# Kernel tuning notes

Hardware: AMD Instinct MI355X
Metric: run time of the kernel (lower is better)

## Reference

```python
import jax, jax.numpy as jnp
import numpy as np

T, NINP, NSTATE, NCH, NLAYER, NCLASS = 8192, 128, 1024, 4, 3, 10
GH = NSTATE // NCH  # per-channel GRU hidden size
EPS = 1e-5


def setup_inputs() -> dict:
    key = jax.random.key(0)
    ks = jax.random.split(key, 32)
    rn = lambda k, shape, scale: (jax.random.normal(k, shape, jnp.float32) * scale)
    he = lambda k, shape: rn(k, shape, (2.0 / shape[-1]) ** 0.5)
    # log_s per layer/channel: scale = 10**i for channel i
    log_s = jnp.log(10.0 ** jnp.arange(NCH, dtype=jnp.float32))[None, :, None]
    inp = {
        "inputs": rn(ks[0], (T, NINP), 1.0),
        "h0": jnp.zeros((GH,), jnp.float32),
        "yinit_guess": jnp.zeros((T, GH), jnp.float32),
        # encoder MLP (ninp -> nstate -> nstate), he_uniform-like init, zero bias
        "enc_w1": he(ks[1], (NSTATE, NINP)),
        "enc_b1": jnp.zeros((NSTATE,), jnp.float32),
        "enc_w2": he(ks[2], (NSTATE, NSTATE)),
        "enc_b2": jnp.zeros((NSTATE,), jnp.float32),
        # per-layer, per-channel GRU params
        "gru_wih": rn(ks[3], (NLAYER, NCH, 3 * GH, NSTATE), NSTATE ** -0.5),  # lecun_normal
        "gru_whh": rn(ks[4], (NLAYER, NCH, 3 * GH, GH), GH ** -0.5),  # stand-in for orthogonal
        "gru_b": jnp.zeros((NLAYER, NCH, 3 * GH), jnp.float32),
        "gru_bn": jnp.zeros((NLAYER, NCH, GH), jnp.float32),
        "gru_log_s": jnp.broadcast_to(log_s, (NLAYER, NCH, 1)).astype(jnp.float32),
        # per-layer residual MLPs (nstate -> nstate -> nstate)
        "mlp_w1": he(ks[5], (NLAYER, NSTATE, NSTATE)),
        "mlp_b1": jnp.zeros((NLAYER, NSTATE), jnp.float32),
        "mlp_w2": he(ks[6], (NLAYER, NSTATE, NSTATE)),
        "mlp_b2": jnp.zeros((NLAYER, NSTATE), jnp.float32),
        # classifier MLP (nstate -> nstate -> nclass)
        "cls_w1": he(ks[7], (NSTATE, NSTATE)),
        "cls_b1": jnp.zeros((NSTATE,), jnp.float32),
        "cls_w2": he(ks[8], (NCLASS, NSTATE)),
        "cls_b2": jnp.zeros((NCLASS,), jnp.float32),
    }
    return inp


def layernorm(x):  # weightless/bias-less LayerNorm over last dim
    m = jnp.mean(x, axis=-1, keepdims=True)
    v = jnp.var(x, axis=-1, keepdims=True)
    return (x - m) / jnp.sqrt(v + EPS)


def mlp(x, w1, b1, w2, b2):  # eqx.nn.MLP depth=1, relu
    h = jax.nn.relu(x @ w1.T + b1)
    return h @ w2.T + b2


def scale_gru_channel(wih, whh, b, bn, log_s, x, h0):
    # ScaleGRU recurrence: per step hnew = GRU(x_t/s, h); h' = (hnew - h)/s + h.
    # This is the exact fixed point that seq1d (DEER) converges to; yinit_guess
    # only affects convergence speed, not the result.
    s = jnp.exp(jnp.clip(log_s, -10.0, 10.0))[0]
    ig = (x / s) @ wih.T + b  # [T, 3*GH], input gates precomputed (parallel GEMM)

    def step(h, ig_t):
        hg = whh @ h  # [3*GH]
        r = jax.nn.sigmoid(ig_t[:GH] + hg[:GH])
        z = jax.nn.sigmoid(ig_t[GH:2 * GH] + hg[GH:2 * GH])
        n = jnp.tanh(ig_t[2 * GH:] + r * (hg[2 * GH:] + bn))
        hnew = n + z * (h - n)  # equinox GRUCell output
        hout = (hnew - h) / s + h  # ScaleGRU rescaling
        return hout, hout

    _, ys = jax.lax.scan(step, h0, ig)
    return ys  # [T, GH]


def reference(inputs, h0, yinit_guess, enc_w1, enc_b1, enc_w2, enc_b2,
              gru_wih, gru_whh, gru_b, gru_bn, gru_log_s,
              mlp_w1, mlp_b1, mlp_w2, mlp_b2,
              cls_w1, cls_b1, cls_w2, cls_b2):
    del yinit_guess  # initial guess for the DEER solver; exact solution is independent of it
    x = mlp(inputs, enc_w1, enc_b1, enc_w2, enc_b2)  # encoder: [T, NSTATE]
    run_channels = jax.vmap(scale_gru_channel, in_axes=(0, 0, 0, 0, 0, None, None))
    for i in range(NLAYER):
        xi = layernorm(x)  # norms[i]
        ch = run_channels(gru_wih[i], gru_whh[i], gru_b[i], gru_bn[i],
                          gru_log_s[i], xi, h0)  # [NCH, T, GH]
        y = jnp.transpose(ch, (1, 0, 2)).reshape(T, NSTATE)  # concat channels on last dim
        y = layernorm(y + xi)  # norms[i+1]
        x = mlp(y, mlp_w1[i], mlp_b1[i], mlp_w2[i], mlp_b2[i]) + y
    return mlp(x, cls_w1, cls_b1, cls_w2, cls_b2)  # [T, NCLASS]
```

## Files before the change

### kernel.cpp

```cpp
#include <hip/hip_runtime.h>

#define T_SEQ  8192
#define NST    1024
#define GHH    256
#define LD_IG  3072
#define C_CH   1024
#define NCHUNK 8
#define NDIAG  10

typedef _Float16 half8 __attribute__((ext_vector_type(8)));
typedef float f32x4 __attribute__((ext_vector_type(4)));

#define MFMA16(a, b, c) __builtin_amdgcn_mfma_f32_16x16x32_f16(a, b, c, 0, 0, 0)

__device__ __forceinline__ float sigmoid_f(float x) {
  return 1.0f / (1.0f + __expf(-x));
}
__device__ __forceinline__ float tanh_f(float x) {
  float ax = fabsf(x);
  float e = __expf(-2.0f * ax);
  float t = (1.0f - e) / (1.0f + e);
  return copysignf(t, x);
}

__global__ __launch_bounds__(256) void prep_whh(const float* __restrict__ whh,
                                                half8* __restrict__ wB)
{
  const int idx = blockIdx.x * 256 + threadIdx.x;
  const int lc  = idx / 24576;
  const int rem = idx - lc * 24576;
  const int g_id = rem >> 6, l = rem & 63;
  const int nb = g_id >> 3, kc = g_id & 7;
  const int g = nb >> 4, ub = nb & 15;
  const int n = l & 15, kg = l >> 4;
  const int row = g * 256 + ub * 16 + n;
  const int col = kc * 32 + kg * 8;
  const float* src = whh + (size_t)lc * 196608 + (size_t)row * 256 + col;
  float4 x0 = *reinterpret_cast<const float4*>(src);
  float4 x1 = *reinterpret_cast<const float4*>(src + 4);
  half8 o;
  o[0] = (_Float16)x0.x; o[1] = (_Float16)x0.y;
  o[2] = (_Float16)x0.z; o[3] = (_Float16)x0.w;
  o[4] = (_Float16)x1.x; o[5] = (_Float16)x1.y;
  o[6] = (_Float16)x1.z; o[7] = (_Float16)x1.w;
  wB[idx] = o;
}

__global__ __launch_bounds__(256) void cvt_to_h(const float* __restrict__ src,
                                                _Float16* __restrict__ dst, int n8)
{
  const int i = blockIdx.x * 256 + threadIdx.x;
  if (i >= n8) return;
  float4 a = reinterpret_cast<const float4*>(src)[2 * i];
  float4 b = reinterpret_cast<const float4*>(src)[2 * i + 1];
  half8 o;
  o[0] = (_Float16)a.x; o[1] = (_Float16)a.y; o[2] = (_Float16)a.z; o[3] = (_Float16)a.w;
  o[4] = (_Float16)b.x; o[5] = (_Float16)b.y; o[6] = (_Float16)b.z; o[7] = (_Float16)b.w;
  reinterpret_cast<half8*>(dst)[i] = o;
}

template<int EPI, bool RELU>
__global__ __launch_bounds__(256) void gemm_h(
    const float* __restrict__ A, const _Float16* __restrict__ Wh,
    const float* __restrict__ bias, const float* __restrict__ R,
    float* __restrict__ C, int M, int N, int K,
    const float* __restrict__ log_s)
{
  __shared__ _Float16 As[64][40];
  __shared__ _Float16 Ws[64][40];
  const int t = threadIdx.x;
  const int bm = blockIdx.x * 64, bn = blockIdx.y * 64;
  const int wave = t >> 6, l = t & 63;
  const int wm = (wave & 1) * 32, wn = (wave >> 1) * 32;
  const int sr = t >> 2, sc = (t & 3) * 8;
  const int fr = l & 15, fk = (l >> 4) * 8;

  f32x4 acc00 = {0.f, 0.f, 0.f, 0.f}, acc01 = acc00, acc10 = acc00, acc11 = acc00;

  const float* Ap     = A  + (size_t)(bm + sr) * K + sc;
  const _Float16* Wp  = Wh + (size_t)(bn + sr) * K + sc;

  for (int k0 = 0; k0 < K; k0 += 32) {
    float4 a0 = *reinterpret_cast<const float4*>(Ap + k0);
    float4 a1 = *reinterpret_cast<const float4*>(Ap + k0 + 4);
    half8 av;
    av[0] = (_Float16)a0.x; av[1] = (_Float16)a0.y;
    av[2] = (_Float16)a0.z; av[3] = (_Float16)a0.w;
    av[4] = (_Float16)a1.x; av[5] = (_Float16)a1.y;
    av[6] = (_Float16)a1.z; av[7] = (_Float16)a1.w;
    *reinterpret_cast<half8*>(&As[sr][sc]) = av;
    *reinterpret_cast<half8*>(&Ws[sr][sc]) =
        *reinterpret_cast<const half8*>(Wp + k0);
    __syncthreads();
    half8 af0 = *reinterpret_cast<const half8*>(&As[wm + fr][fk]);
    half8 af1 = *reinterpret_cast<const half8*>(&As[wm + 16 + fr][fk]);
    half8 bf0 = *reinterpret_cast<const half8*>(&Ws[wn + fr][fk]);
    half8 bf1 = *reinterpret_cast<const half8*>(&Ws[wn + 16 + fr][fk]);
    acc00 = MFMA16(af0, bf0, acc00);
    acc01 = MFMA16(af0, bf1, acc01);
    acc10 = MFMA16(af1, bf0, acc10);
    acc11 = MFMA16(af1, bf1, acc11);
    __syncthreads();
  }

#define EPI_STORE(ac, mi, ni) { \
    const int n_ = bn + wn + (ni) * 16 + fr; \
    const float bv = bias[n_]; \
    float sc_ = 1.f; \
    if (EPI == 1) { \
      float lsv = log_s[n_ / 768]; \
      lsv = fminf(fmaxf(lsv, -10.f), 10.f); \
      sc_ = __expf(-lsv); \
    } \
    _Pragma("unroll") \
    for (int q = 0; q < 4; ++q) { \
      const int m_ = bm + wm + (mi) * 16 + (l >> 4) * 4 + q; \
      float v = ac[q]; \
      if (EPI == 1) v *= sc_; \
      v += bv; \
      if (EPI == 2) v += R[(size_t)m_ * N + n_]; \
      if (RELU) v = fmaxf(v, 0.f); \
      C[(size_t)m_ * N + n_] = v; \
    } }
  EPI_STORE(acc00, 0, 0) EPI_STORE(acc01, 0, 1)
  EPI_STORE(acc10, 1, 0) EPI_STORE(acc11, 1, 1)
#undef EPI_STORE
}

template<bool ADD>
__global__ __launch_bounds__(256) void ln_kernel(const float* __restrict__ X,
                                                 const float* __restrict__ Yad,
                                                 float* __restrict__ O)
{
  const int row = blockIdx.x, t = threadIdx.x;
  float4 v = reinterpret_cast<const float4*>(X + (size_t)row * NST)[t];
  if (ADD) {
    float4 w = reinterpret_cast<const float4*>(Yad + (size_t)row * NST)[t];
    v.x += w.x; v.y += w.y; v.z += w.z; v.w += w.w;
  }
  float s  = v.x + v.y + v.z + v.w;
  float ss = v.x * v.x + v.y * v.y + v.z * v.z + v.w * v.w;
#pragma unroll
  for (int m = 1; m < 64; m <<= 1) {
    s  += __shfl_xor(s, m, 64);
    ss += __shfl_xor(ss, m, 64);
  }
  __shared__ float ps[4], pss[4];
  const int wv = t >> 6;
  if ((t & 63) == 0) { ps[wv] = s; pss[wv] = ss; }
  __syncthreads();
  s  = ps[0] + ps[1] + ps[2] + ps[3];
  ss = pss[0] + pss[1] + pss[2] + pss[3];
  const float mean = s * (1.f / 1024.f);
  const float var  = ss * (1.f / 1024.f) - mean * mean;
  const float rstd = rsqrtf(var + 1e-5f);
  v.x = (v.x - mean) * rstd; v.y = (v.y - mean) * rstd;
  v.z = (v.z - mean) * rstd; v.w = (v.w - mean) * rstd;
  reinterpret_cast<float4*>(O + (size_t)row * NST)[t] = v;
}

__global__ __launch_bounds__(256) void ln2_kernel(const float* __restrict__ Y,
                                                  const float* __restrict__ X,
                                                  float* __restrict__ O)
{
  const int row = blockIdx.x, t = threadIdx.x;
  const int wv = t >> 6;
  __shared__ float ps[4], pss[4], ps2[4], pss2[4];

  float4 xv = reinterpret_cast<const float4*>(X + (size_t)row * NST)[t];
  float s  = xv.x + xv.y + xv.z + xv.w;
  float ss = xv.x * xv.x + xv.y * xv.y + xv.z * xv.z + xv.w * xv.w;
#pragma unroll
  for (int m = 1; m < 64; m <<= 1) {
    s += __shfl_xor(s, m, 64); ss += __shfl_xor(ss, m, 64);
  }
  if ((t & 63) == 0) { ps[wv] = s; pss[wv] = ss; }
  __syncthreads();
  s = ps[0] + ps[1] + ps[2] + ps[3];
  ss = pss[0] + pss[1] + pss[2] + pss[3];
  float mean = s * (1.f / 1024.f);
  float var  = ss * (1.f / 1024.f) - mean * mean;
  float rstd = rsqrtf(var + 1e-5f);

  float4 yv = reinterpret_cast<const float4*>(Y + (size_t)row * NST)[t];
  float4 v;
  v.x = yv.x + (xv.x - mean) * rstd;
  v.y = yv.y + (xv.y - mean) * rstd;
  v.z = yv.z + (xv.z - mean) * rstd;
  v.w = yv.w + (xv.w - mean) * rstd;

  s  = v.x + v.y + v.z + v.w;
  ss = v.x * v.x + v.y * v.y + v.z * v.z + v.w * v.w;
#pragma unroll
  for (int m = 1; m < 64; m <<= 1) {
    s += __shfl_xor(s, m, 64); ss += __shfl_xor(ss, m, 64);
  }
  if ((t & 63) == 0) { ps2[wv] = s; pss2[wv] = ss; }
  __syncthreads();
  s = ps2[0] + ps2[1] + ps2[2] + ps2[3];
  ss = pss2[0] + pss2[1] + pss2[2] + pss2[3];
  mean = s * (1.f / 1024.f);
  var  = ss * (1.f / 1024.f) - mean * mean;
  rstd = rsqrtf(var + 1e-5f);
  v.x = (v.x - mean) * rstd; v.y = (v.y - mean) * rstd;
  v.z = (v.z - mean) * rstd; v.w = (v.w - mean) * rstd;
  reinterpret_cast<float4*>(O + (size_t)row * NST)[t] = v;
}

#define SCAN_BAR() asm volatile("s_waitcnt lgkmcnt(0)\n\ts_barrier" ::: "memory")

#define DECLB(i) half8 B##i##_0, B##i##_1, B##i##_2, B##i##_3, \
                       B##i##_4, B##i##_5, B##i##_6, B##i##_7;
#define LOADBn(i, nb) \
  B##i##_0 = wpB[((nb)*8+0)*64]; B##i##_1 = wpB[((nb)*8+1)*64]; \
  B##i##_2 = wpB[((nb)*8+2)*64]; B##i##_3 = wpB[((nb)*8+3)*64]; \
  B##i##_4 = wpB[((nb)*8+4)*64]; B##i##_5 = wpB[((nb)*8+5)*64]; \
  B##i##_6 = wpB[((nb)*8+6)*64]; B##i##_7 = wpB[((nb)*8+7)*64];

#define KCSTEP(kc) { \
  half8 a = hp[(kc) * 4]; \
  a0 = MFMA16(a, B0_##kc, a0); a1 = MFMA16(a, B1_##kc, a1); \
  a2 = MFMA16(a, B2_##kc, a2); a3 = MFMA16(a, B3_##kc, a3); \
  a4 = MFMA16(a, B4_##kc, a4); a5 = MFMA16(a, B5_##kc, a5); }

__global__ __attribute__((amdgpu_flat_work_group_size(512, 512)))
void scan_diag(
    const half8* __restrict__ wB,
    const float* __restrict__ gbn,
    const float* __restrict__ gls,
    const float* __restrict__ igb,
    const float* __restrict__ h0,
    float* __restrict__ hst,
    float* __restrict__ yb,
    int d)
{
  const int lidx = blockIdx.x >> 2;
  const int ch   = blockIdx.x & 3;
  const int c    = d - lidx;
  if (c < 0 || c >= NCHUNK) return;

  const int j = threadIdx.x;
  const int w = j >> 6, l = j & 63;
  const int lc = lidx * 4 + ch;
  const float* igc = igb + (size_t)lidx * (C_CH * LD_IG) + ch * 768;
  float* yc        = yb + (size_t)lidx * (C_CH * NST) + ch * GHH;

  const half8* wpB = wB + (size_t)lc * 24576 + l;
  DECLB(0) DECLB(1) DECLB(2) DECLB(3) DECLB(4) DECLB(5)
  LOADBn(0, w)      LOADBn(1, w + 8)  LOADBn(2, w + 16)
  LOADBn(3, w + 24) LOADBn(4, w + 32) LOADBn(5, w + 40)

  __shared__ __align__(16) _Float16 hsl[2][GHH];

  const bool glane = (l < 32);
  const bool hi    = (l & 16) != 0;
  const int u = 16 * w + (l & 15) + (hi ? 128 : 0);

  float ls = gls[lc];
  ls = fminf(fmaxf(ls, -10.f), 10.f);
  const float inv_s = __expf(-ls);
  float bnu = 0.f, h = 0.f, ir = 0.f, iz = 0.f, in_ = 0.f;
  if (glane) {
    h   = (c == 0) ? h0[u] : hst[lc * GHH + u];
    bnu = gbn[lc * GHH + u];
    hsl[0][u] = (_Float16)h;
    ir = igc[u]; iz = igc[256 + u]; in_ = igc[512 + u];
  }
  SCAN_BAR();

  for (int t = 0; t < C_CH; ++t) {
    float nr = 0.f, nz = 0.f, nn = 0.f;
    if (glane && t + 1 < C_CH) {
      const float* p = igc + (size_t)(t + 1) * LD_IG;
      nr = p[u]; nz = p[256 + u]; nn = p[512 + u];
    }
    const half8* hp = reinterpret_cast<const half8*>(hsl[t & 1]) + (l >> 4);
    f32x4 a0 = {0.f, 0.f, 0.f, 0.f}, a1 = a0, a2 = a0, a3 = a0, a4 = a0, a5 = a0;
    KCSTEP(0) KCSTEP(1) KCSTEP(2) KCSTEP(3)
    KCSTEP(4) KCSTEP(5) KCSTEP(6) KCSTEP(7)
    if (glane) {
      const float pr = hi ? a1[0] : a0[0];
      const float pz = hi ? a3[0] : a2[0];
      const float pn = hi ? a5[0] : a4[0];
      const float rg = sigmoid_f(ir + pr);
      const float zg = sigmoid_f(iz + pz);
      const float ng = tanh_f(in_ + rg * (pn + bnu));
      const float hw = ng + zg * (h - ng);
      h = (hw - h) * inv_s + h;
      yc[(size_t)t * NST + u] = h;
      hsl[(t + 1) & 1][u] = (_Float16)h;
    }
    SCAN_BAR();
    ir = nr; iz = nz; in_ = nn;
  }
  if (glane) hst[lc * GHH + u] = h;
}

__global__ __launch_bounds__(256) void gemv_cls(const float* __restrict__ A,
                                                const float* __restrict__ W,
                                                const float* __restrict__ b,
                                                float* __restrict__ out)
{
  const int m = blockIdx.x, t = threadIdx.x;
  float4 a = reinterpret_cast<const float4*>(A + (size_t)m * NST)[t];
  float p[10];
#pragma unroll
  for (int n = 0; n < 10; ++n) {
    float4 w = reinterpret_cast<const float4*>(W + (size_t)n * NST)[t];
    p[n] = a.x * w.x + a.y * w.y + a.z * w.z + a.w * w.w;
  }
#pragma unroll
  for (int n = 0; n < 10; ++n)
#pragma unroll
    for (int msk = 1; msk < 64; msk <<= 1) p[n] += __shfl_xor(p[n], msk, 64);
  __shared__ float red[4][10];
  const int wv = t >> 6;
  if ((t & 63) == 0) {
#pragma unroll
    for (int n = 0; n < 10; ++n) red[wv][n] = p[n];
  }
  __syncthreads();
  if (t < 10) {
    float v = red[0][t] + red[1][t] + red[2][t] + red[3][t] + b[t];
    out[(size_t)m * 10 + t] = v;
  }
}

extern "C" void kernel_launch(void* const* d_in, const int* in_sizes, int n_in,
                              void* d_out, int out_size, void* d_ws, size_t ws_size,
                              hipStream_t stream) {
  const float* inputs = (const float*)d_in[0];
  const float* h0     = (const float*)d_in[1];
  const float* enc_w1 = (const float*)d_in[3];
  const float* enc_b1 = (const float*)d_in[4];
  const float* enc_w2 = (const float*)d_in[5];
  const float* enc_b2 = (const float*)d_in[6];
  const float* gwih   = (const float*)d_in[7];
  const float* gwhh   = (const float*)d_in[8];
  const float* gb     = (const float*)d_in[9];
  const float* gbn    = (const float*)d_in[10];
  const float* gls    = (const float*)d_in[11];
  const float* mw1    = (const float*)d_in[12];
  const float* mb1    = (const float*)d_in[13];
  const float* mw2    = (const float*)d_in[14];
  const float* mb2    = (const float*)d_in[15];
  const float* cw1    = (const float*)d_in[16];
  const float* cb1    = (const float*)d_in[17];
  const float* cw2    = (const float*)d_in[18];
  const float* cb2    = (const float*)d_in[19];
  float* out = (float*)d_out;

  char* ws = (char*)d_ws;
  float* x0    = (float*)(ws);
  float* xr1   = (float*)(ws + 33554432ull);
  float* xr2   = (float*)(ws + 41943040ull);
  float* igbuf = (float*)(ws + 50331648ull);
  half8* gw16  = (half8*)(ws + 88080384ull);
  float* bufY  = (float*)(ws + 92798976ull);
  float* bufYn = (float*)(ws + 105381888ull);
  float* bufH  = (float*)(ws + 109576192ull);
  float* xitmp = (float*)(ws + 113770496ull);
  float* xf    = (float*)(ws + 117964800ull);
  float* clsH  = (float*)(ws + 122159104ull);
  float* hst   = (float*)(ws + 126353408ull);
  _Float16* wf = (_Float16*)(ws + 126365696ull);

  _Float16* wh_enc1 = wf;
  _Float16* wh_enc2 = wf + 131072;
  _Float16* wh_wih  = wf + 1179648;
  _Float16* wh_mw1  = wf + 10616832;
  _Float16* wh_mw2  = wf + 13762560;
  _Float16* wh_cw1  = wf + 16908288;

  const dim3 blk(256);
  const dim3 g_enc(8192 / 64, 1024 / 64);
  const dim3 g_ig(C_CH / 64, 3072 / 64);
  const dim3 g_mlp(C_CH / 64, 1024 / 64);

  auto xptr = [&](int lth, int c) -> float* {
    if (lth == 0) return x0 + (size_t)c * C_CH * NST;
    float* base = (lth == 1) ? xr1 : xr2;
    return base + (size_t)(c & 1) * C_CH * NST;
  };

  prep_whh<<<dim3(1152), blk, 0, stream>>>(gwhh, gw16);
  cvt_to_h<<<dim3(64),   blk, 0, stream>>>(enc_w1, wh_enc1, 16384);
  cvt_to_h<<<dim3(512),  blk, 0, stream>>>(enc_w2, wh_enc2, 131072);
  cvt_to_h<<<dim3(4608), blk, 0, stream>>>(gwih,   wh_wih,  1179648);
  cvt_to_h<<<dim3(1536), blk, 0, stream>>>(mw1,    wh_mw1,  393216);
  cvt_to_h<<<dim3(1536), blk, 0, stream>>>(mw2,    wh_mw2,  393216);
  cvt_to_h<<<dim3(512),  blk, 0, stream>>>(cw1,    wh_cw1,  131072);

  gemm_h<0, true ><<<g_enc, blk, 0, stream>>>(inputs, wh_enc1, enc_b1, nullptr,
                                              (float*)igbuf, 8192, 1024, 128, nullptr);
  gemm_h<0, false><<<g_enc, blk, 0, stream>>>((float*)igbuf, wh_enc2, enc_b2, nullptr,
                                              x0, 8192, 1024, 1024, nullptr);

  for (int d = 0; d < NDIAG; ++d) {
    for (int lth = 0; lth < 3; ++lth) {
      const int c = d - lth;
      if (c < 0 || c >= NCHUNK) continue;
      ln_kernel<false><<<dim3(C_CH), blk, 0, stream>>>(xptr(lth, c), nullptr, xitmp);
      gemm_h<1, false><<<g_ig, blk, 0, stream>>>(
          xitmp, wh_wih + (size_t)lth * 3145728, gb + (size_t)lth * 3072,
          nullptr, igbuf + (size_t)lth * C_CH * LD_IG, C_CH, 3072, 1024,
          gls + (size_t)lth * 4);
    }
    scan_diag<<<dim3(12), dim3(512), 0, stream>>>(gw16, gbn, gls, igbuf,
                                                  h0, hst, bufY, d);
    for (int lth = 0; lth < 3; ++lth) {
      const int c = d - lth;
      if (c < 0 || c >= NCHUNK) continue;
      ln2_kernel<<<dim3(C_CH), blk, 0, stream>>>(
          bufY + (size_t)lth * C_CH * NST, xptr(lth, c), bufYn);
      gemm_h<0, true ><<<g_mlp, blk, 0, stream>>>(
          bufYn, wh_mw1 + (size_t)lth * 1048576, mb1 + (size_t)lth * 1024,
          nullptr, bufH, C_CH, 1024, 1024, nullptr);
      float* xnext = (lth < 2) ? xptr(lth + 1, c) : xf;
      gemm_h<2, false><<<g_mlp, blk, 0, stream>>>(
          bufH, wh_mw2 + (size_t)lth * 1048576, mb2 + (size_t)lth * 1024,
          bufYn, xnext, C_CH, 1024, 1024, nullptr);
      if (lth == 2) {
        gemm_h<0, true><<<g_mlp, blk, 0, stream>>>(
            xf, wh_cw1, cb1, nullptr, clsH, C_CH, 1024, 1024, nullptr);
        gemv_cls<<<dim3(C_CH), blk, 0, stream>>>(clsH, cw2, cb2,
                                                 out + (size_t)c * C_CH * 10);
      }
    }
  }
}
```

Baseline: 12.04 ms.

## Batch per-layer diagonal kernels into single launches over a layer grid dimension

Merges the per-layer LayerNorm, input-gate GEMM, and MLP GEMMs of each diagonal step into single batched launches, with blockIdx.z selecting the layer and an early exit for layers inactive at that diagonal. This removes up to three launches per stage and gives each GEMM up to three times as many blocks, so the GPU is better filled at chunk size 1024. Workspace buffers are re-laid out into a contiguous per-layer stack, and ln2 now writes in place into bufY. The cost is idle blocks launched for inactive layers on the edge diagonals.

```diff
diff --git a/kernel.cpp b/kernel.cpp
--- a/kernel.cpp
+++ b/kernel.cpp
@@ -21,6 +21,12 @@
   float e = __expf(-2.0f * ax);
   float t = (1.0f - e) / (1.0f + e);
   return copysignf(t, x);
+}
+
+__device__ __forceinline__ const float* xin_ptr(const float* x0, const float* xn,
+                                                int z, int c) {
+  return (z == 0) ? x0 + (size_t)c * C_CH * NST
+                  : xn + (size_t)(z - 1) * C_CH * NST;
 }
 
 __global__ __launch_bounds__(256) void prep_whh(const float* __restrict__ whh,
@@ -60,16 +66,13 @@
 }
 
 template<int EPI, bool RELU>
-__global__ __launch_bounds__(256) void gemm_h(
+__device__ __forceinline__ void gemm_body(
     const float* __restrict__ A, const _Float16* __restrict__ Wh,
     const float* __restrict__ bias, const float* __restrict__ R,
-    float* __restrict__ C, int M, int N, int K,
-    const float* __restrict__ log_s)
-{
-  __shared__ _Float16 As[64][40];
-  __shared__ _Float16 Ws[64][40];
+    float* __restrict__ C, int N, int K, const float* __restrict__ log_s,
+    int bm, int bn, _Float16 (*As)[40], _Float16 (*Ws)[40])
+{
   const int t = threadIdx.x;
-  const int bm = blockIdx.x * 64, bn = blockIdx.y * 64;
   const int wave = t >> 6, l = t & 63;
   const int wm = (wave & 1) * 32, wn = (wave >> 1) * 32;
   const int sr = t >> 2, sc = (t & 3) * 8;
@@ -127,23 +130,55 @@
 #undef EPI_STORE
 }
 
-template<bool ADD>
-__global__ __launch_bounds__(256) void ln_kernel(const float* __restrict__ X,
-                                                 const float* __restrict__ Yad,
-                                                 float* __restrict__ O)
-{
-  const int row = blockIdx.x, t = threadIdx.x;
-  float4 v = reinterpret_cast<const float4*>(X + (size_t)row * NST)[t];
-  if (ADD) {
-    float4 w = reinterpret_cast<const float4*>(Yad + (size_t)row * NST)[t];
-    v.x += w.x; v.y += w.y; v.z += w.z; v.w += w.w;
-  }
+template<int EPI, bool RELU>
+__global__ __launch_bounds__(256) void gemm_h(
+    const float* __restrict__ A, const _Float16* __restrict__ Wh,
+    const float* __restrict__ bias, const float* __restrict__ R,
+    float* __restrict__ C, int M, int N, int K,
+    const float* __restrict__ log_s)
+{
+  __shared__ _Float16 As[64][40];
+  __shared__ _Float16 Ws[64][40];
+  gemm_body<EPI, RELU>(A, Wh, bias, R, C, N, K, log_s,
+                       blockIdx.x * 64, blockIdx.y * 64, As, Ws);
+}
+
+template<int EPI, bool RELU>
+__global__ __launch_bounds__(256) void gemm_b(
+    const float* __restrict__ Abase, size_t Astride,
+    const _Float16* __restrict__ Wbase, size_t Wstride,
+    const float* __restrict__ bbase, size_t bstride,
+    const float* __restrict__ Rbase, size_t Rstride,
+    float* __restrict__ Cbase, size_t Cstride,
+    int N, int K, const float* __restrict__ lsbase, int d)
+{
+  const int z = blockIdx.z;
+  if ((unsigned)(d - z) >= NCHUNK) return;
+  __shared__ _Float16 As[64][40];
+  __shared__ _Float16 Ws[64][40];
+  gemm_body<EPI, RELU>(Abase + (size_t)z * Astride, Wbase + (size_t)z * Wstride,
+                       bbase + (size_t)z * bstride,
+                       Rbase ? Rbase + (size_t)z * Rstride : nullptr,
+                       Cbase + (size_t)z * Cstride, N, K,
+                       lsbase ? lsbase + (size_t)z * 4 : nullptr,
+                       blockIdx.x * 64, blockIdx.y * 64, As, Ws);
+}
+
+__global__ __launch_bounds__(256) void ln_pre_b(const float* __restrict__ x0,
+                                                const float* __restrict__ xn,
+                                                float* __restrict__ O, int d)
+{
+  const int z = blockIdx.x >> 10, row = blockIdx.x & 1023;
+  const int c = d - z;
+  if ((unsigned)c >= NCHUNK) return;
+  const int t = threadIdx.x;
+  const float* X = xin_ptr(x0, xn, z, c) + (size_t)row * NST;
+  float4 v = reinterpret_cast<const float4*>(X)[t];
   float s  = v.x + v.y + v.z + v.w;
   float ss = v.x * v.x + v.y * v.y + v.z * v.z + v.w * v.w;
 #pragma unroll
   for (int m = 1; m < 64; m <<= 1) {
-    s  += __shfl_xor(s, m, 64);
-    ss += __shfl_xor(ss, m, 64);
+    s += __shfl_xor(s, m, 64); ss += __shfl_xor(ss, m, 64);
   }
   __shared__ float ps[4], pss[4];
   const int wv = t >> 6;
@@ -156,18 +191,25 @@
   const float rstd = rsqrtf(var + 1e-5f);
   v.x = (v.x - mean) * rstd; v.y = (v.y - mean) * rstd;
   v.z = (v.z - mean) * rstd; v.w = (v.w - mean) * rstd;
-  reinterpret_cast<float4*>(O + (size_t)row * NST)[t] = v;
-}
-
-__global__ __launch_bounds__(256) void ln2_kernel(const float* __restrict__ Y,
-                                                  const float* __restrict__ X,
-                                                  float* __restrict__ O)
-{
-  const int row = blockIdx.x, t = threadIdx.x;
+  reinterpret_cast<float4*>(O + ((size_t)z * C_CH + row) * NST)[t] = v;
+}
+
+__global__ __launch_bounds__(256) void ln2_b(float* __restrict__ Y,
+                                             const float* __restrict__ x0,
+                                             const float* __restrict__ xn,
+                                             int d)
+{
+  const int z = blockIdx.x >> 10, row = blockIdx.x & 1023;
+  const int c = d - z;
+  if ((unsigned)c >= NCHUNK) return;
+  const int t = threadIdx.x;
   const int wv = t >> 6;
   __shared__ float ps[4], pss[4], ps2[4], pss2[4];
 
-  float4 xv = reinterpret_cast<const float4*>(X + (size_t)row * NST)[t];
+  const float* X = xin_ptr(x0, xn, z, c) + (size_t)row * NST;
+  float* Yr = Y + ((size_t)z * C_CH + row) * NST;
+
+  float4 xv = reinterpret_cast<const float4*>(X)[t];
   float s  = xv.x + xv.y + xv.z + xv.w;
   float ss = xv.x * xv.x + xv.y * xv.y + xv.z * xv.z + xv.w * xv.w;
 #pragma unroll
@@ -182,7 +224,7 @@
   float var  = ss * (1.f / 1024.f) - mean * mean;
   float rstd = rsqrtf(var + 1e-5f);
 
-  float4 yv = reinterpret_cast<const float4*>(Y + (size_t)row * NST)[t];
+  float4 yv = reinterpret_cast<const float4*>(Yr)[t];
   float4 v;
   v.x = yv.x + (xv.x - mean) * rstd;
   v.y = yv.y + (xv.y - mean) * rstd;
@@ -204,7 +246,7 @@
   rstd = rsqrtf(var + 1e-5f);
   v.x = (v.x - mean) * rstd; v.y = (v.y - mean) * rstd;
   v.z = (v.z - mean) * rstd; v.w = (v.w - mean) * rstd;
-  reinterpret_cast<float4*>(O + (size_t)row * NST)[t] = v;
+  reinterpret_cast<float4*>(Yr)[t] = v;
 }
 
 #define SCAN_BAR() asm volatile("s_waitcnt lgkmcnt(0)\n\ts_barrier" ::: "memory")
@@ -352,16 +394,13 @@
 
   char* ws = (char*)d_ws;
   float* x0    = (float*)(ws);
-  float* xr1   = (float*)(ws + 33554432ull);
-  float* xr2   = (float*)(ws + 41943040ull);
-  float* igbuf = (float*)(ws + 50331648ull);
-  half8* gw16  = (half8*)(ws + 88080384ull);
-  float* bufY  = (float*)(ws + 92798976ull);
-  float* bufYn = (float*)(ws + 105381888ull);
-  float* bufH  = (float*)(ws + 109576192ull);
-  float* xitmp = (float*)(ws + 113770496ull);
-  float* xf    = (float*)(ws + 117964800ull);
-  float* clsH  = (float*)(ws + 122159104ull);
+  float* xn    = (float*)(ws + 33554432ull);
+  float* xitmp = (float*)(ws + 46137344ull);
+  float* clsH  = xitmp;
+  float* igbuf = (float*)(ws + 58720256ull);
+  half8* gw16  = (half8*)(ws + 96468992ull);
+  float* bufY  = (float*)(ws + 101187584ull);
+  float* bufH  = (float*)(ws + 113770496ull);
   float* hst   = (float*)(ws + 126353408ull);
   _Float16* wf = (_Float16*)(ws + 126365696ull);
 
@@ -374,14 +413,9 @@
 
   const dim3 blk(256);
   const dim3 g_enc(8192 / 64, 1024 / 64);
-  const dim3 g_ig(C_CH / 64, 3072 / 64);
+  const dim3 g_ig_b(C_CH / 64, 3072 / 64, 3);
+  const dim3 g_mlp_b(C_CH / 64, 1024 / 64, 3);
   const dim3 g_mlp(C_CH / 64, 1024 / 64);
-
-  auto xptr = [&](int lth, int c) -> float* {
-    if (lth == 0) return x0 + (size_t)c * C_CH * NST;
-    float* base = (lth == 1) ? xr1 : xr2;
-    return base + (size_t)(c & 1) * C_CH * NST;
-  };
 
   prep_whh<<<dim3(1152), blk, 0, stream>>>(gwhh, gw16);
   cvt_to_h<<<dim3(64),   blk, 0, stream>>>(enc_w1, wh_enc1, 16384);
@@ -397,35 +431,25 @@
                                               x0, 8192, 1024, 1024, nullptr);
 
   for (int d = 0; d < NDIAG; ++d) {
-    for (int lth = 0; lth < 3; ++lth) {
-      const int c = d - lth;
-      if (c < 0 || c >= NCHUNK) continue;
-      ln_kernel<false><<<dim3(C_CH), blk, 0, stream>>>(xptr(lth, c), nullptr, xitmp);
-      gemm_h<1, false><<<g_ig, blk, 0, stream>>>(
-          xitmp, wh_wih + (size_t)lth * 3145728, gb + (size_t)lth * 3072,
-          nullptr, igbuf + (size_t)lth * C_CH * LD_IG, C_CH, 3072, 1024,
-          gls + (size_t)lth * 4);
-    }
+    ln_pre_b<<<dim3(3 * C_CH), blk, 0, stream>>>(x0, xn, xitmp, d);
+    gemm_b<1, false><<<g_ig_b, blk, 0, stream>>>(
+        xitmp, (size_t)C_CH * NST, wh_wih, 3145728ull, gb, 3072ull,
+        nullptr, 0ull, igbuf, (size_t)C_CH * LD_IG, 3072, 1024, gls, d);
     scan_diag<<<dim3(12), dim3(512), 0, stream>>>(gw16, gbn, gls, igbuf,
                                                   h0, hst, bufY, d);
-    for (int lth = 0; lth < 3; ++lth) {
-      const int c = d - lth;
-      if (c < 0 || c >= NCHUNK) continue;
-      ln2_kernel<<<dim3(C_CH), blk, 0, stream>>>(
-          bufY + (size_t)lth * C_CH * NST, xptr(lth, c), bufYn);
-      gemm_h<0, true ><<<g_mlp, blk, 0, stream>>>(
-          bufYn, wh_mw1 + (size_t)lth * 1048576, mb1 + (size_t)lth * 1024,
-          nullptr, bufH, C_CH, 1024, 1024, nullptr);
-      float* xnext = (lth < 2) ? xptr(lth + 1, c) : xf;
-      gemm_h<2, false><<<g_mlp, blk, 0, stream>>>(
-          bufH, wh_mw2 + (size_t)lth * 1048576, mb2 + (size_t)lth * 1024,
-          bufYn, xnext, C_CH, 1024, 1024, nullptr);
-      if (lth == 2) {
-        gemm_h<0, true><<<g_mlp, blk, 0, stream>>>(
-            xf, wh_cw1, cb1, nullptr, clsH, C_CH, 1024, 1024, nullptr);
-        gemv_cls<<<dim3(C_CH), blk, 0, stream>>>(clsH, cw2, cb2,
-                                                 out + (size_t)c * C_CH * 10);
-      }
+    ln2_b<<<dim3(3 * C_CH), blk, 0, stream>>>(bufY, x0, xn, d);
+    gemm_b<0, true ><<<g_mlp_b, blk, 0, stream>>>(
+        bufY, (size_t)C_CH * NST, wh_mw1, 1048576ull, mb1, 1024ull,
+        nullptr, 0ull, bufH, (size_t)C_CH * NST, 1024, 1024, nullptr, d);
+    gemm_b<2, false><<<g_mlp_b, blk, 0, stream>>>(
+        bufH, (size_t)C_CH * NST, wh_mw2, 1048576ull, mb2, 1024ull,
+        bufY, (size_t)C_CH * NST, xn, (size_t)C_CH * NST, 1024, 1024, nullptr, d);
+    const int c2 = d - 2;
+    if (0 <= c2 && c2 < NCHUNK) {
+      gemm_h<0, true><<<g_mlp, blk, 0, stream>>>(
+          xn + 2ull * C_CH * NST, wh_cw1, cb1, nullptr, clsH, C_CH, 1024, 1024, nullptr);
+      gemv_cls<<<dim3(C_CH), blk, 0, stream>>>(clsH, cw2, cb2,
+                                               out + (size_t)c2 * C_CH * 10);
     }
   }
 }
```

Result: faster. 11.41 ms (-5.2%).
